# Performance work log

Hardware: AMD Instinct MI355X
Metric: run time of the kernel (lower is better)

## Reference

```python
import jax, jax.numpy as jnp
import numpy as np

N_NODES = 100000


def setup_inputs() -> dict:
    key = jax.random.key(0)
    ks = jax.random.split(key, 4)
    x = jax.random.normal(ks[0], (N_NODES, 128), dtype=jnp.float32)
    edge_index = jax.random.randint(ks[1], (2, 1600000), 0, N_NODES, dtype=jnp.int64)
    W1 = jax.random.normal(ks[2], (128, 64), dtype=jnp.float32) * (1.0 / np.sqrt(128))
    b1 = jnp.zeros((64,), dtype=jnp.float32)
    W2 = jax.random.normal(ks[3], (64, 64), dtype=jnp.float32) * (1.0 / np.sqrt(64))
    b2 = jnp.zeros((64,), dtype=jnp.float32)
    return {"x": x, "edge_index": edge_index, "W1": W1, "b1": b1, "W2": W2, "b2": b2}


def reference(x, edge_index, W1, b1, W2, b2):
    N = x.shape[0]
    loop = jnp.arange(N, dtype=edge_index.dtype)
    src = jnp.concatenate([edge_index[0], loop])  # [E+N] sources (incl. self-loops)
    dst = jnp.concatenate([edge_index[1], loop])  # [E+N] targets
    # symmetric GCN normalization: deg counts edge weights (all 1) at target nodes
    deg = jax.ops.segment_sum(jnp.ones_like(src, dtype=x.dtype), dst, num_segments=N)
    dinv = jnp.where(deg > 0, jax.lax.rsqrt(deg), 0.0)
    norm = (dinv[src] * dinv[dst])[:, None]  # [E+N, 1]

    def gcn_conv(h, W, b):
        h = h @ W                                   # dense transform [N, out]
        msg = h[src] * norm                         # gather + normalize [E+N, out]
        agg = jax.ops.segment_sum(msg, dst, num_segments=N)  # scatter-add
        return agg + b

    h = jax.nn.gelu(gcn_conv(x, W1, b1), approximate=False)  # torch nn.GELU = exact erf
    return gcn_conv(h, W2, b2)
```

## Files before the change

kernel.cpp:

```cpp
#include <hip/hip_runtime.h>
#include <math.h>

#define N_NODES 100000
#define N_EDGES 1600000
#define NBUK 782
#define BCAP 2600
#define BINCHUNK 4096

typedef unsigned short u16;
typedef u16 u16x4 __attribute__((ext_vector_type(4)));
typedef u16 u16x8 __attribute__((ext_vector_type(8)));
typedef short s16x8 __attribute__((ext_vector_type(8)));
typedef float f32x4 __attribute__((ext_vector_type(4)));

__device__ __forceinline__ float bf2f(u16 u) {
    union { unsigned i; float f; } v; v.i = ((unsigned)u) << 16; return v.f;
}
__device__ __forceinline__ u16 f2bf(float f) {
    union { float f; unsigned i; } v; v.f = f;
    return (u16)((v.i + 0x7FFFu + ((v.i >> 16) & 1u)) >> 16);
}

__global__ __launch_bounds__(256) void k_bin(const int* __restrict__ src,
                                             const int* __restrict__ dst,
                                             int* bucketCursor,
                                             unsigned int* __restrict__ bins) {
    __shared__ int lcnt[NBUK];
    __shared__ int lbase[NBUK];
    const int t = threadIdx.x;
    for (int i = t; i < NBUK; i += 256) lcnt[i] = 0;
    __syncthreads();

    const int e0 = blockIdx.x * BINCHUNK + t * 16;
    int4 s4[4], d4[4];
    int bkt[16], rnk[16];
    const bool valid = e0 < N_EDGES;
    if (valid) {
        #pragma unroll
        for (int k = 0; k < 4; ++k) {
            s4[k] = *(const int4*)(src + e0 + 4 * k);
            d4[k] = *(const int4*)(dst + e0 + 4 * k);
        }
        #pragma unroll
        for (int k = 0; k < 4; ++k) {
            int dd[4] = { d4[k].x, d4[k].y, d4[k].z, d4[k].w };
            #pragma unroll
            for (int j = 0; j < 4; ++j) {
                int b = dd[j] >> 7;
                bkt[4 * k + j] = b;
                rnk[4 * k + j] = atomicAdd(&lcnt[b], 1);
            }
        }
    }
    __syncthreads();
    for (int i = t; i < NBUK; i += 256)
        if (lcnt[i] > 0) lbase[i] = atomicAdd(&bucketCursor[i], lcnt[i]);
    __syncthreads();
    if (valid) {
        #pragma unroll
        for (int k = 0; k < 4; ++k) {
            int ss[4] = { s4[k].x, s4[k].y, s4[k].z, s4[k].w };
            int dd[4] = { d4[k].x, d4[k].y, d4[k].z, d4[k].w };
            #pragma unroll
            for (int j = 0; j < 4; ++j) {
                int i = 4 * k + j;
                unsigned w = ((unsigned)(dd[j] & 127) << 17) | (unsigned)ss[j];
                bins[(size_t)bkt[i] * BCAP + lbase[bkt[i]] + rnk[i]] = w;
            }
        }
    }
}

__global__ __launch_bounds__(256) void k_bscan(const int* __restrict__ bucketCursor,
                                               int* __restrict__ gBase,
                                               int* __restrict__ row_start) {
    __shared__ int sd[256];
    const int t = threadIdx.x;
    const int idx0 = t * 4;
    int v0 = (idx0 + 0 < NBUK) ? bucketCursor[idx0 + 0] : 0;
    int v1 = (idx0 + 1 < NBUK) ? bucketCursor[idx0 + 1] : 0;
    int v2 = (idx0 + 2 < NBUK) ? bucketCursor[idx0 + 2] : 0;
    int v3 = (idx0 + 3 < NBUK) ? bucketCursor[idx0 + 3] : 0;
    int s0 = v0, s1 = s0 + v1, s2 = s1 + v2, s3 = s2 + v3;
    sd[t] = s3;
    __syncthreads();
    #pragma unroll
    for (int off = 1; off < 256; off <<= 1) {
        int x = (t >= off) ? sd[t - off] : 0;
        __syncthreads();
        sd[t] += x;
        __syncthreads();
    }
    int excl = (t > 0) ? sd[t - 1] : 0;
    if (idx0 + 0 < NBUK) gBase[idx0 + 0] = excl;
    if (idx0 + 1 < NBUK) gBase[idx0 + 1] = excl + s0;
    if (idx0 + 2 < NBUK) gBase[idx0 + 2] = excl + s1;
    if (idx0 + 3 < NBUK) gBase[idx0 + 3] = excl + s2;
    if (t == 0) row_start[N_NODES] = N_EDGES;
}

__global__ __launch_bounds__(256) void k_build(const unsigned int* __restrict__ bins,
                                               const int* __restrict__ bucketCursor,
                                               const int* __restrict__ gBase,
                                               int* __restrict__ row_start,
                                               float* __restrict__ dinv,
                                               int* __restrict__ csr_src) {
    __shared__ int cnt[128];
    __shared__ int ps[128];
    __shared__ int cur[128];
    const int b = blockIdx.x;
    const int t = threadIdx.x;
    const int bcnt = bucketCursor[b];
    const int gb = gBase[b];
    const unsigned int* mybins = bins + (size_t)b * BCAP;

    if (t < 128) cnt[t] = 0;
    __syncthreads();
    for (int i = t; i < bcnt; i += 256)
        atomicAdd(&cnt[mybins[i] >> 17], 1);
    __syncthreads();
    if (t < 128) ps[t] = cnt[t];
    __syncthreads();
    #pragma unroll
    for (int off = 1; off < 128; off <<= 1) {
        int x = (t >= off && t < 128) ? ps[t - off] : 0;
        __syncthreads();
        if (t < 128) ps[t] += x;
        __syncthreads();
    }
    if (t < 128) {
        int excl = (t > 0) ? ps[t - 1] : 0;
        cur[t] = excl;
        int node = (b << 7) + t;
        if (node < N_NODES) {
            row_start[node] = gb + excl;
            dinv[node] = rsqrtf((float)(cnt[t] + 1));
        }
    }
    __syncthreads();
    for (int i = t; i < bcnt; i += 256) {
        unsigned w = mybins[i];
        int dl = w >> 17;
        int s = (int)(w & 0x1FFFFu);
        int p = atomicAdd(&cur[dl], 1);
        csr_src[gb + p] = s;
    }
}

__global__ __launch_bounds__(256) void k_gemm1(const float* __restrict__ X,
                                               const float* __restrict__ W,
                                               const float* __restrict__ dinv,
                                               u16* __restrict__ H) {
    __shared__ u16 sxh[64 * 128];
    __shared__ u16 sxl[64 * 128];
    __shared__ u16 wth[64 * 128];
    __shared__ u16 wtl[64 * 128];
    const int t = threadIdx.x;
    const int blk = blockIdx.x;

    {
        const float4* Xv = (const float4*)X;
        #pragma unroll
        for (int i = 0; i < 8; ++i) {
            int idx = i * 256 + t;
            int row = idx >> 5;
            int k4  = (idx & 31) << 2;
            int grow = blk * 64 + row;
            float4 v = make_float4(0.f, 0.f, 0.f, 0.f);
            if (grow < N_NODES) v = Xv[(size_t)grow * 32 + (idx & 31)];
            float f[4] = { v.x, v.y, v.z, v.w };
            u16x4 hv, lv;
            #pragma unroll
            for (int j = 0; j < 4; ++j) {
                u16 h = f2bf(f[j]);
                hv[j] = h;
                lv[j] = f2bf(f[j] - bf2f(h));
            }
            int byte = (row * 256 + k4 * 2) ^ ((row & 7) << 4);
            *(u16x4*)((char*)sxh + byte) = hv;
            *(u16x4*)((char*)sxl + byte) = lv;
        }
    }
    {
        const float4* Wv = (const float4*)W;
        #pragma unroll
        for (int i = 0; i < 8; ++i) {
            int idx = i * 256 + t;
            int k  = idx >> 4;
            int c0 = (idx & 15) << 2;
            float4 v = Wv[idx];
            float f[4] = { v.x, v.y, v.z, v.w };
            #pragma unroll
            for (int j = 0; j < 4; ++j) {
                int c = c0 + j;
                int byte = (c * 256 + k * 2) ^ ((c & 7) << 4);
                u16 h = f2bf(f[j]);
                *(u16*)((char*)wth + byte) = h;
                *(u16*)((char*)wtl + byte) = f2bf(f[j] - bf2f(h));
            }
        }
    }
    __syncthreads();

    const int lane = t & 63;
    const int w    = t >> 6;
    const int l16  = lane & 15;
    const int kg   = lane >> 4;
    f32x4 acc[4];
    #pragma unroll
    for (int nt = 0; nt < 4; ++nt)
        #pragma unroll
        for (int j = 0; j < 4; ++j) acc[nt][j] = 0.f;

    const int arow = w * 16 + l16;
    const int aswz = (arow & 7) << 4;
    #pragma unroll
    for (int kt = 0; kt < 4; ++kt) {
        const int koff = kt * 64 + kg * 16;
        s16x8 ah = *(const s16x8*)((const char*)sxh + ((arow * 256 + koff) ^ aswz));
        s16x8 al = *(const s16x8*)((const char*)sxl + ((arow * 256 + koff) ^ aswz));
        #pragma unroll
        for (int nt = 0; nt < 4; ++nt) {
            const int c = nt * 16 + l16;
            const int wb = (c * 256 + koff) ^ ((c & 7) << 4);
            s16x8 bh = *(const s16x8*)((const char*)wth + wb);
            s16x8 bl = *(const s16x8*)((const char*)wtl + wb);
            acc[nt] = __builtin_amdgcn_mfma_f32_16x16x32_bf16(ah, bh, acc[nt], 0, 0, 0);
            acc[nt] = __builtin_amdgcn_mfma_f32_16x16x32_bf16(ah, bl, acc[nt], 0, 0, 0);
            acc[nt] = __builtin_amdgcn_mfma_f32_16x16x32_bf16(al, bh, acc[nt], 0, 0, 0);
        }
    }
    const int rbase = blk * 64 + w * 16 + kg * 4;
    #pragma unroll
    for (int reg = 0; reg < 4; ++reg) {
        int row = rbase + reg;
        float di = (row < N_NODES) ? dinv[row] : 0.f;
        #pragma unroll
        for (int nt = 0; nt < 4; ++nt)
            __builtin_nontemporal_store(f2bf(acc[nt][reg] * di),
                                        &H[(size_t)row * 64 + nt * 16 + l16]);
    }
}

__global__ __launch_bounds__(256) void k_gemm2(const u16* __restrict__ Xb,
                                               const float* __restrict__ W,
                                               const float* __restrict__ dinv,
                                               u16* __restrict__ H) {
    __shared__ u16 sxb[64 * 64];
    __shared__ u16 wth[64 * 64];
    __shared__ u16 wtl[64 * 64];
    const int t = threadIdx.x;
    const int blk = blockIdx.x;

    {
        const u16x8* Xv = (const u16x8*)Xb;
        #pragma unroll
        for (int i = 0; i < 2; ++i) {
            int idx = i * 256 + t;
            int row = idx >> 3;
            int k0  = (idx & 7) << 3;
            int grow = blk * 64 + row;
            u16x8 v;
            #pragma unroll
            for (int j = 0; j < 8; ++j) v[j] = 0;
            if (grow < N_NODES) v = Xv[(size_t)grow * 8 + (idx & 7)];
            int byte = (row * 128 + k0 * 2) ^ ((row & 7) << 4);
            *(u16x8*)((char*)sxb + byte) = v;
        }
    }
    {
        const float4* Wv = (const float4*)W;
        #pragma unroll
        for (int i = 0; i < 4; ++i) {
            int idx = i * 256 + t;
            int k  = idx >> 4;
            int c0 = (idx & 15) << 2;
            float4 v = Wv[idx];
            float f[4] = { v.x, v.y, v.z, v.w };
            #pragma unroll
            for (int j = 0; j < 4; ++j) {
                int c = c0 + j;
                int byte = (c * 128 + k * 2) ^ ((c & 7) << 4);
                u16 h = f2bf(f[j]);
                *(u16*)((char*)wth + byte) = h;
                *(u16*)((char*)wtl + byte) = f2bf(f[j] - bf2f(h));
            }
        }
    }
    __syncthreads();

    const int lane = t & 63;
    const int w    = t >> 6;
    const int l16  = lane & 15;
    const int kg   = lane >> 4;
    f32x4 acc[4];
    #pragma unroll
    for (int nt = 0; nt < 4; ++nt)
        #pragma unroll
        for (int j = 0; j < 4; ++j) acc[nt][j] = 0.f;

    const int arow = w * 16 + l16;
    const int aswz = (arow & 7) << 4;
    #pragma unroll
    for (int kt = 0; kt < 2; ++kt) {
        const int koff = kt * 64 + kg * 16;
        s16x8 a = *(const s16x8*)((const char*)sxb + ((arow * 128 + koff) ^ aswz));
        #pragma unroll
        for (int nt = 0; nt < 4; ++nt) {
            const int c = nt * 16 + l16;
            const int wb = (c * 128 + koff) ^ ((c & 7) << 4);
            s16x8 bh = *(const s16x8*)((const char*)wth + wb);
            s16x8 bl = *(const s16x8*)((const char*)wtl + wb);
            acc[nt] = __builtin_amdgcn_mfma_f32_16x16x32_bf16(a, bh, acc[nt], 0, 0, 0);
            acc[nt] = __builtin_amdgcn_mfma_f32_16x16x32_bf16(a, bl, acc[nt], 0, 0, 0);
        }
    }
    const int rbase = blk * 64 + w * 16 + kg * 4;
    #pragma unroll
    for (int reg = 0; reg < 4; ++reg) {
        int row = rbase + reg;
        float di = (row < N_NODES) ? dinv[row] : 0.f;
        #pragma unroll
        for (int nt = 0; nt < 4; ++nt)
            __builtin_nontemporal_store(f2bf(acc[nt][reg] * di),
                                        &H[(size_t)row * 64 + nt * 16 + l16]);
    }
}

template <bool GELU>
__global__ __launch_bounds__(256) void k_aggregate(const u16* __restrict__ hs,
                                                   const int* __restrict__ csr_src,
                                                   const int* __restrict__ row_start,
                                                   const float* __restrict__ dinv,
                                                   const float* __restrict__ b,
                                                   void* __restrict__ outraw) {
    const int t = threadIdx.x;
    const int lane = t & 63;
    const int node = __builtin_amdgcn_readfirstlane(blockIdx.x * 4 + (t >> 6));
    const int jS = __builtin_amdgcn_readfirstlane(row_start[node]);
    const int jE = __builtin_amdgcn_readfirstlane(row_start[node + 1]);
    const int deg = jE - jS;
    const u16* __restrict__ colp = hs + lane;

    int raw[32];
    #pragma unroll
    for (int i = 0; i < 32; ++i)
        raw[i] = __builtin_amdgcn_readfirstlane(csr_src[jS + i]);

    float acc = bf2f(colp[(size_t)node << 6]);
    u16 v[32];
    #pragma unroll
    for (int i = 0; i < 32; ++i) {
        int idx = (i < deg) ? raw[i] : N_NODES;
        v[i] = colp[(size_t)(unsigned)idx << 6];
    }
    #pragma unroll
    for (int i = 0; i < 32; ++i) acc += bf2f(v[i]);

    if (deg > 32) {
        for (int j = jS + 32; j < jE; ++j) {
            int idx = __builtin_amdgcn_readfirstlane(csr_src[j]);
            acc += bf2f(colp[(size_t)(unsigned)idx << 6]);
        }
    }

    float r = dinv[node] * acc + b[lane];
    if (GELU) {
        r = 0.5f * r * (1.0f + erff(r * 0.70710678118654752f));
        ((u16*)outraw)[((size_t)node << 6) + lane] = f2bf(r);
    } else {
        ((float*)outraw)[((size_t)node << 6) + lane] = r;
    }
}

extern "C" void kernel_launch(void* const* d_in, const int* in_sizes, int n_in,
                              void* d_out, int out_size, void* d_ws, size_t ws_size,
                              hipStream_t stream) {
    const float* x  = (const float*)d_in[0];
    const int* edge = (const int*)d_in[1];
    const float* W1 = (const float*)d_in[2];
    const float* b1 = (const float*)d_in[3];
    const float* W2 = (const float*)d_in[4];
    const float* b2 = (const float*)d_in[5];
    float* out = (float*)d_out;

    const int* src = edge;
    const int* dst = edge + N_EDGES;

    char* ws = (char*)d_ws;
    int*   bucketCursor = (int*)(ws);
    int*   gBase        = (int*)(ws + 4096);
    int*   row_start    = (int*)(ws + 8192);
    float* dinv         = (float*)(ws + 408576);
    int*   csr_src      = (int*)(ws + 808960);
    u16*   hsb          = (u16*)(ws + 7209088);
    unsigned int* bins  = (unsigned int*)hsb;
    u16*   out1b        = (u16*)(ws + 20013184);

    const int nBlkBin  = (N_EDGES + BINCHUNK - 1) / BINCHUNK;
    const int nBlkGemm = (N_NODES + 63) / 64;
    const int nBlkAgg  = N_NODES / 4;

    hipMemsetAsync(bucketCursor, 0, NBUK * sizeof(int), stream);
    k_bin<<<nBlkBin, 256, 0, stream>>>(src, dst, bucketCursor, bins);
    k_bscan<<<1, 256, 0, stream>>>(bucketCursor, gBase, row_start);
    k_build<<<NBUK, 256, 0, stream>>>(bins, bucketCursor, gBase, row_start, dinv, csr_src);

    k_gemm1<<<nBlkGemm, 256, 0, stream>>>(x, W1, dinv, hsb);
    k_aggregate<true><<<nBlkAgg, 256, 0, stream>>>(hsb, csr_src, row_start, dinv, b1, out1b);

    k_gemm2<<<nBlkGemm, 256, 0, stream>>>(out1b, W2, dinv, hsb);
    k_aggregate<false><<<nBlkAgg, 256, 0, stream>>>(hsb, csr_src, row_start, dinv, b2, out);
}
```

Baseline: 167.5 us.

## Fuse layer-1 aggregation with layer-2 GEMM and pre-split weights once

Merges the first aggregation (with GELU) into the second GEMM kernel, so each block aggregates its 64 rows straight into shared memory and runs the MFMA transform without writing and re-reading an intermediate bf16 buffer. Also adds a small kernel that splits W1/W2 into hi/lo bf16 in swizzled layout once, instead of every GEMM block converting them. The cost is fewer blocks (64 rows per block instead of 4), each wave walking 16 nodes in sequence, which may cut latency hiding in the gather, plus one extra kernel launch.

```diff
diff --git a/kernel.cpp b/kernel.cpp
--- a/kernel.cpp
+++ b/kernel.cpp
@@ -147,8 +147,37 @@
     }
 }
 
+__global__ __launch_bounds__(256) void k_wsplit(const float* __restrict__ W1,
+                                                const float* __restrict__ W2,
+                                                u16* __restrict__ w1pre,
+                                                u16* __restrict__ w2pre) {
+    const int t = threadIdx.x;
+    #pragma unroll
+    for (int i = 0; i < 32; ++i) {
+        int e = i * 256 + t;
+        int k = e >> 6, c = e & 63;
+        float f = W1[e];
+        u16 h = f2bf(f);
+        u16 l = f2bf(f - bf2f(h));
+        int byte = (c * 256 + k * 2) ^ ((c & 7) << 4);
+        *(u16*)((char*)w1pre + byte) = h;
+        *(u16*)((char*)w1pre + 16384 + byte) = l;
+    }
+    #pragma unroll
+    for (int i = 0; i < 16; ++i) {
+        int e = i * 256 + t;
+        int k = e >> 6, c = e & 63;
+        float f = W2[e];
+        u16 h = f2bf(f);
+        u16 l = f2bf(f - bf2f(h));
+        int byte = (c * 128 + k * 2) ^ ((c & 7) << 4);
+        *(u16*)((char*)w2pre + byte) = h;
+        *(u16*)((char*)w2pre + 8192 + byte) = l;
+    }
+}
+
 __global__ __launch_bounds__(256) void k_gemm1(const float* __restrict__ X,
-                                               const float* __restrict__ W,
+                                               const u16* __restrict__ w1pre,
                                                const float* __restrict__ dinv,
                                                u16* __restrict__ H) {
     __shared__ u16 sxh[64 * 128];
@@ -182,23 +211,13 @@
         }
     }
     {
-        const float4* Wv = (const float4*)W;
-        #pragma unroll
-        for (int i = 0; i < 8; ++i) {
-            int idx = i * 256 + t;
-            int k  = idx >> 4;
-            int c0 = (idx & 15) << 2;
-            float4 v = Wv[idx];
-            float f[4] = { v.x, v.y, v.z, v.w };
-            #pragma unroll
-            for (int j = 0; j < 4; ++j) {
-                int c = c0 + j;
-                int byte = (c * 256 + k * 2) ^ ((c & 7) << 4);
-                u16 h = f2bf(f[j]);
-                *(u16*)((char*)wth + byte) = h;
-                *(u16*)((char*)wtl + byte) = f2bf(f[j] - bf2f(h));
-            }
-        }
+        const u16x8* G = (const u16x8*)w1pre;
+        u16x8* Lh = (u16x8*)wth;
+        u16x8* Ll = (u16x8*)wtl;
+        #pragma unroll
+        for (int i = 0; i < 4; ++i) Lh[i * 256 + t] = G[i * 256 + t];
+        #pragma unroll
+        for (int i = 0; i < 4; ++i) Ll[i * 256 + t] = G[1024 + i * 256 + t];
     }
     __syncthreads();
 
@@ -242,57 +261,72 @@
     }
 }
 
-__global__ __launch_bounds__(256) void k_gemm2(const u16* __restrict__ Xb,
-                                               const float* __restrict__ W,
-                                               const float* __restrict__ dinv,
-                                               u16* __restrict__ H) {
+__global__ __launch_bounds__(256) void k_agg1g2(const u16* __restrict__ hs,
+                                                const int* __restrict__ csr_src,
+                                                const int* __restrict__ row_start,
+                                                const float* __restrict__ dinv,
+                                                const float* __restrict__ b1,
+                                                const u16* __restrict__ w2pre,
+                                                u16* __restrict__ H2) {
     __shared__ u16 sxb[64 * 64];
     __shared__ u16 wth[64 * 64];
     __shared__ u16 wtl[64 * 64];
     const int t = threadIdx.x;
     const int blk = blockIdx.x;
+    const int w = t >> 6;
+    const int lane = t & 63;
 
     {
-        const u16x8* Xv = (const u16x8*)Xb;
-        #pragma unroll
-        for (int i = 0; i < 2; ++i) {
-            int idx = i * 256 + t;
-            int row = idx >> 3;
-            int k0  = (idx & 7) << 3;
-            int grow = blk * 64 + row;
-            u16x8 v;
-            #pragma unroll
-            for (int j = 0; j < 8; ++j) v[j] = 0;
-            if (grow < N_NODES) v = Xv[(size_t)grow * 8 + (idx & 7)];
-            int byte = (row * 128 + k0 * 2) ^ ((row & 7) << 4);
-            *(u16x8*)((char*)sxb + byte) = v;
-        }
-    }
-    {
-        const float4* Wv = (const float4*)W;
-        #pragma unroll
-        for (int i = 0; i < 4; ++i) {
-            int idx = i * 256 + t;
-            int k  = idx >> 4;
-            int c0 = (idx & 15) << 2;
-            float4 v = Wv[idx];
-            float f[4] = { v.x, v.y, v.z, v.w };
-            #pragma unroll
-            for (int j = 0; j < 4; ++j) {
-                int c = c0 + j;
-                int byte = (c * 128 + k * 2) ^ ((c & 7) << 4);
-                u16 h = f2bf(f[j]);
-                *(u16*)((char*)wth + byte) = h;
-                *(u16*)((char*)wtl + byte) = f2bf(f[j] - bf2f(h));
+        const u16x8* G = (const u16x8*)w2pre;
+        u16x8* Lh = (u16x8*)wth;
+        u16x8* Ll = (u16x8*)wtl;
+        #pragma unroll
+        for (int i = 0; i < 2; ++i) Lh[i * 256 + t] = G[i * 256 + t];
+        #pragma unroll
+        for (int i = 0; i < 2; ++i) Ll[i * 256 + t] = G[512 + i * 256 + t];
+    }
+
+    const u16* __restrict__ colp = hs + lane;
+    const float bb = b1[lane];
+    #pragma unroll 1
+    for (int i = 0; i < 16; ++i) {
+        const int row = w * 16 + i;
+        const int node = blk * 64 + row;
+        const int byte = (row * 128 + lane * 2) ^ ((row & 7) << 4);
+        if (node < N_NODES) {
+            const int jS = __builtin_amdgcn_readfirstlane(row_start[node]);
+            const int jE = __builtin_amdgcn_readfirstlane(row_start[node + 1]);
+            const int deg = jE - jS;
+            int raw[32];
+            #pragma unroll
+            for (int k = 0; k < 32; ++k)
+                raw[k] = __builtin_amdgcn_readfirstlane(csr_src[jS + k]);
+            float acc = bf2f(colp[(size_t)node << 6]);
+            u16 v[32];
+            #pragma unroll
+            for (int k = 0; k < 32; ++k) {
+                int idx = (k < deg) ? raw[k] : N_NODES;
+                v[k] = colp[(size_t)(unsigned)idx << 6];
             }
-        }
-    }
-    __syncthreads();
-
-    const int lane = t & 63;
-    const int w    = t >> 6;
-    const int l16  = lane & 15;
-    const int kg   = lane >> 4;
+            #pragma unroll
+            for (int k = 0; k < 32; ++k) acc += bf2f(v[k]);
+            if (deg > 32) {
+                for (int j = jS + 32; j < jE; ++j) {
+                    int idx = __builtin_amdgcn_readfirstlane(csr_src[j]);
+                    acc += bf2f(colp[(size_t)(unsigned)idx << 6]);
+                }
+            }
+            float r = dinv[node] * acc + bb;
+            r = 0.5f * r * (1.0f + erff(r * 0.70710678118654752f));
+            *(u16*)((char*)sxb + byte) = f2bf(r);
+        } else {
+            *(u16*)((char*)sxb + byte) = 0;
+        }
+    }
+    __syncthreads();
+
+    const int l16 = lane & 15;
+    const int kg  = lane >> 4;
     f32x4 acc[4];
     #pragma unroll
     for (int nt = 0; nt < 4; ++nt)
@@ -323,17 +357,16 @@
         #pragma unroll
         for (int nt = 0; nt < 4; ++nt)
             __builtin_nontemporal_store(f2bf(acc[nt][reg] * di),
-                                        &H[(size_t)row * 64 + nt * 16 + l16]);
-    }
-}
-
-template <bool GELU>
-__global__ __launch_bounds__(256) void k_aggregate(const u16* __restrict__ hs,
-                                                   const int* __restrict__ csr_src,
-                                                   const int* __restrict__ row_start,
-                                                   const float* __restrict__ dinv,
-                                                   const float* __restrict__ b,
-                                                   void* __restrict__ outraw) {
+                                        &H2[(size_t)row * 64 + nt * 16 + l16]);
+    }
+}
+
+__global__ __launch_bounds__(256) void k_aggregate2(const u16* __restrict__ hs,
+                                                    const int* __restrict__ csr_src,
+                                                    const int* __restrict__ row_start,
+                                                    const float* __restrict__ dinv,
+                                                    const float* __restrict__ b,
+                                                    float* __restrict__ out) {
     const int t = threadIdx.x;
     const int lane = t & 63;
     const int node = __builtin_amdgcn_readfirstlane(blockIdx.x * 4 + (t >> 6));
@@ -364,13 +397,7 @@
         }
     }
 
-    float r = dinv[node] * acc + b[lane];
-    if (GELU) {
-        r = 0.5f * r * (1.0f + erff(r * 0.70710678118654752f));
-        ((u16*)outraw)[((size_t)node << 6) + lane] = f2bf(r);
-    } else {
-        ((float*)outraw)[((size_t)node << 6) + lane] = r;
-    }
+    out[((size_t)node << 6) + lane] = dinv[node] * acc + b[lane];
 }
 
 extern "C" void kernel_launch(void* const* d_in, const int* in_sizes, int n_in,
@@ -395,20 +422,23 @@
     int*   csr_src      = (int*)(ws + 808960);
     u16*   hsb          = (u16*)(ws + 7209088);
     unsigned int* bins  = (unsigned int*)hsb;
-    u16*   out1b        = (u16*)(ws + 20013184);
+    u16*   hsb2         = (u16*)(ws + 20013184);
+    u16*   w1pre        = (u16*)(ws + 32817280);
+    u16*   w2pre        = (u16*)(ws + 32850048);
 
     const int nBlkBin  = (N_EDGES + BINCHUNK - 1) / BINCHUNK;
     const int nBlkGemm = (N_NODES + 63) / 64;
     const int nBlkAgg  = N_NODES / 4;
 
     hipMemsetAsync(bucketCursor, 0, NBUK * sizeof(int), stream);
+    k_wsplit<<<1, 256, 0, stream>>>(W1, W2, w1pre, w2pre);
     k_bin<<<nBlkBin, 256, 0, stream>>>(src, dst, bucketCursor, bins);
     k_bscan<<<1, 256, 0, stream>>>(bucketCursor, gBase, row_start);
     k_build<<<NBUK, 256, 0, stream>>>(bins, bucketCursor, gBase, row_start, dinv, csr_src);
 
-    k_gemm1<<<nBlkGemm, 256, 0, stream>>>(x, W1, dinv, hsb);
-    k_aggregate<true><<<nBlkAgg, 256, 0, stream>>>(hsb, csr_src, row_start, dinv, b1, out1b);
-
-    k_gemm2<<<nBlkGemm, 256, 0, stream>>>(out1b, W2, dinv, hsb);
-    k_aggregate<false><<<nBlkAgg, 256, 0, stream>>>(hsb, csr_src, row_start, dinv, b2, out);
-}
+    k_gemm1<<<nBlkGemm, 256, 0, stream>>>(x, w1pre, dinv, hsb);
+
+    k_agg1g2<<<nBlkGemm, 256, 0, stream>>>(hsb, csr_src, row_start, dinv, b1, w2pre, hsb2);
+
+    k_aggregate2<<<nBlkAgg, 256, 0, stream>>>(hsb2, csr_src, row_start, dinv, b2, out);
+}
```

Result: slower. 191.7 us (+14.4%).
